# Performance work log

Measured on AMD Instinct MI355X. Metric: run time of the kernel, lower is better.

Reference implementation:

```python
import jax, jax.numpy as jnp
import numpy as np

N_INPUT, N_HIDDEN, N_OUTPUT = 64, 1024, 64
B, T = 128, 512

def setup_inputs() -> dict:
    key = jax.random.key(0)
    ks = jax.random.split(key, 8)
    s_in = 1.0 / np.sqrt(N_INPUT)
    s_h = 1.0 / np.sqrt(N_HIDDEN)
    return {
        "x": jax.random.normal(ks[0], (B, T, N_INPUT), jnp.float32),
        "enc_w": jax.random.uniform(ks[1], (N_HIDDEN, N_INPUT), jnp.float32, -s_in, s_in),
        "enc_b": jax.random.uniform(ks[2], (N_HIDDEN,), jnp.float32, -s_in, s_in),
        "rec_w": jax.random.uniform(ks[3], (N_HIDDEN, N_HIDDEN), jnp.float32, -s_h, s_h),
        "fgt_w": jax.random.uniform(ks[4], (N_HIDDEN, N_HIDDEN), jnp.float32, -s_h, s_h),
        "dec_w": jax.random.uniform(ks[5], (N_OUTPUT, N_HIDDEN), jnp.float32, -s_h, s_h),
        "dec_b": jax.random.uniform(ks[6], (N_OUTPUT,), jnp.float32, -s_h, s_h),
        "hinit_w": jax.random.uniform(ks[7], (N_HIDDEN, 1), jnp.float32, -1.0, 1.0),
        "hinit_b": jax.random.uniform(jax.random.fold_in(key, 9), (N_HIDDEN,), jnp.float32, -1.0, 1.0),
    }

def softsign(x):
    return x / (1.0 + jnp.abs(x))

def reference(x, enc_w, enc_b, rec_w, fgt_w, dec_w, dec_b, hinit_w, hinit_b):
    # x: [B, T, I] -> time-major [T, B, I]
    xt = jnp.transpose(x, (1, 0, 2))
    # hidden_init(ones(B,1)) = ones @ hinit_w^T + b = broadcast of column sum
    hidden0 = jnp.broadcast_to(hinit_w[:, 0] + hinit_b, (x.shape[0], hinit_b.shape[0]))
    # Precompute encoder projection for all timesteps (same math, one big GEMM)
    enc_all = jnp.einsum('tbi,hi->tbh', xt, enc_w) + enc_b  # [T, B, H]

    def step(hidden, enc_t):
        forget = jax.nn.sigmoid(hidden @ fgt_w.T)
        hidden_new = softsign(enc_t + hidden @ rec_w.T)
        hidden = (1.0 - forget) * hidden + forget * hidden_new
        out_t = hidden @ dec_w.T + dec_b
        return hidden, out_t

    hidden, output = jax.lax.scan(step, hidden0, enc_all)
    return output, hidden  # output: [T, B, O], hidden: [B, H]
```

## Files before the change

kernel.cpp:

```cpp
#include <hip/hip_runtime.h>

typedef unsigned short u16;

#define NWG 256
#define NT  256
#define TS  512
#define HD  1024
#define BS  128
#define NI  64
#define NO  64
#define XR  16
#define CC  32
#define RCP 17

typedef __attribute__((ext_vector_type(8))) short bf16x8;
typedef __attribute__((ext_vector_type(4))) float f32x4;

__device__ __forceinline__ float bf2f(u16 u) {
    union { unsigned int i; float f; } v; v.i = ((unsigned int)u) << 16; return v.f;
}
__device__ __forceinline__ u16 f2bf(float f) {
    union { float fl; unsigned int i; } v; v.fl = f;
    unsigned int x = v.i;
    return (u16)((x + 0x7fffu + ((x >> 16) & 1u)) >> 16);
}
__device__ __forceinline__ float ldv(const void* p, size_t i, bool isf32) {
    return isf32 ? ((const float*)p)[i] : bf2f(((const u16*)p)[i]);
}

__device__ __forceinline__ unsigned l2_atomic_add(unsigned* p, unsigned v) {
    unsigned old;
    asm volatile("global_atomic_add %0, %1, %2, off sc0\n\t"
                 "s_waitcnt vmcnt(0)"
                 : "=&v"(old) : "v"(p), "v"(v) : "memory");
    return old;
}
__device__ __forceinline__ void l2_atomic_add_nr(unsigned* p, unsigned v) {
    asm volatile("global_atomic_add %0, %1, off" :: "v"(p), "v"(v) : "memory");
}

__device__ __forceinline__ void load_a_frags(const u16* ap, bf16x8* a) {
    asm volatile(
        "global_load_dwordx4 %0, %8, off sc0\n\t"
        "global_load_dwordx4 %1, %8, off offset:64 sc0\n\t"
        "global_load_dwordx4 %2, %8, off offset:128 sc0\n\t"
        "global_load_dwordx4 %3, %8, off offset:192 sc0\n\t"
        "global_load_dwordx4 %4, %8, off offset:256 sc0\n\t"
        "global_load_dwordx4 %5, %8, off offset:320 sc0\n\t"
        "global_load_dwordx4 %6, %8, off offset:384 sc0\n\t"
        "global_load_dwordx4 %7, %8, off offset:448 sc0\n\t"
        "s_waitcnt vmcnt(0)"
        : "=&v"(a[0]), "=&v"(a[1]), "=&v"(a[2]), "=&v"(a[3]),
          "=&v"(a[4]), "=&v"(a[5]), "=&v"(a[6]), "=&v"(a[7])
        : "v"(ap) : "memory");
}

#define MB_STRIDE 16

__global__ __launch_bounds__(NT)
void arnn_xcd(const void* __restrict__ xv,
              const void* __restrict__ encwv,
              const void* __restrict__ encbv,
              const void* __restrict__ recwv,
              const void* __restrict__ fgtwv,
              const void* __restrict__ decwv,
              const void* __restrict__ decbv,
              const void* __restrict__ hinitwv,
              const void* __restrict__ hinitbv,
              void* __restrict__ outv,
              u16* __restrict__ h0buf,
              u16* __restrict__ h1buf,
              unsigned* __restrict__ tickets,
              unsigned* __restrict__ mboxes)
{
    __shared__ short WB[132 * 64 * 8];
    __shared__ float redC[4 * 5 * 16 * RCP];
    __shared__ float hst[XR * CC];
    __shared__ float encbS[CC];
    __shared__ float decbLS[16];
    __shared__ unsigned s_xcd, s_slot;
    __shared__ int s_f32;

    const int tid  = threadIdx.x;
    const int wave = tid >> 6;
    const int lane = tid & 63;
    const int m    = lane & 15;
    const int quad = lane >> 4;

    if (tid == 0) {
        unsigned xcc;
        asm volatile("s_getreg_b32 %0, hwreg(HW_REG_XCC_ID, 0, 4)" : "=s"(xcc));
        xcc &= 7u;
        unsigned slot = l2_atomic_add(tickets + xcc * 16, 1u);
        s_xcd = xcc;
        s_slot = slot & 31u;
        s_f32 = 0;
    }
    __syncthreads();
    {
        float v = bf2f(((const u16*)recwv)[tid]);
        if (!(v >= -1.0f && v <= 1.0f)) s_f32 = 1;
    }
    __syncthreads();
    const bool isf32 = (s_f32 != 0);
    const int xcd  = (int)s_xcd;
    const int slot = (int)s_slot;
    const int b0   = xcd * XR;
    const int j0   = slot * CC;
    const int dt   = slot & 3;
    unsigned* mbX   = mboxes + (size_t)xcd * 32 * MB_STRIDE;
    unsigned* mbOwn = mbX + slot * MB_STRIDE;

    for (int idx = tid; idx < 132 * 64; idx += NT) {
        int ksg = idx >> 6, l = idx & 63, n = l & 15, q = l >> 4;
        int tile, ksl;
        if (ksg < 34)       { tile = 0; ksl = ksg; }
        else if (ksg < 68)  { tile = 1; ksl = ksg - 34; }
        else if (ksg < 100) { tile = 2; ksl = ksg - 68; }
        else                { tile = 3; ksl = ksg - 100; }
        int j = j0 + ((tile & 1) << 4) + n;
        bf16x8 v;
        if (!isf32) {
            const u16* src;
            if (tile < 2) src = (ksl < 32) ? (const u16*)recwv + (size_t)j * HD + ksl * 32 + q * 8
                                           : (const u16*)encwv + (size_t)j * NI + (ksl - 32) * 32 + q * 8;
            else          src = (const u16*)fgtwv + (size_t)j * HD + ksl * 32 + q * 8;
            v = *(const bf16x8*)src;
        } else {
            const float* src;
            if (tile < 2) src = (ksl < 32) ? (const float*)recwv + (size_t)j * HD + ksl * 32 + q * 8
                                           : (const float*)encwv + (size_t)j * NI + (ksl - 32) * 32 + q * 8;
            else          src = (const float*)fgtwv + (size_t)j * HD + ksl * 32 + q * 8;
            #pragma unroll
            for (int i = 0; i < 8; ++i) v[i] = (short)f2bf(src[i]);
        }
        *(bf16x8*)&WB[idx * 8] = v;
    }
    __syncthreads();

    bf16x8 Breg[2][8];
    #pragma unroll
    for (int ks = 0; ks < 8; ++ks) {
        int kb = wave * 8 + ks;
        Breg[0][ks] = *(const bf16x8*)&WB[((0  + kb) * 64 + lane) * 8];
        Breg[1][ks] = *(const bf16x8*)&WB[((34 + kb) * 64 + lane) * 8];
    }
    bf16x8 Ereg[2];
    if (wave < 2) {
        Ereg[0] = *(const bf16x8*)&WB[((32 + wave) * 64 + lane) * 8];
        Ereg[1] = *(const bf16x8*)&WB[((34 + 32 + wave) * 64 + lane) * 8];
    }
    bf16x8 dfr[8];
    {
        int o = 16 * dt + m;
        #pragma unroll
        for (int ks = 0; ks < 8; ++ks) {
            int kb = wave * 256 + ks * 32 + quad * 8;
            if (!isf32) dfr[ks] = *(const bf16x8*)((const u16*)decwv + (size_t)o * HD + kb);
            else {
                const float* src = (const float*)decwv + (size_t)o * HD + kb;
                #pragma unroll
                for (int i = 0; i < 8; ++i) dfr[ks][i] = (short)f2bf(src[i]);
            }
        }
    }
    if (tid < CC) encbS[tid] = ldv(encbv, j0 + tid, isf32);
    if (tid < 16) decbLS[tid] = ldv(decbv, 16 * dt + tid, isf32);
    for (int e = tid; e < XR * CC; e += NT) {
        int r = e >> 5, c = e & 31;
        float v = ldv(hinitwv, j0 + c, isf32) + ldv(hinitbv, j0 + c, isf32);
        hst[e] = v;
        h0buf[(size_t)(b0 + r) * HD + j0 + c] = f2bf(v);
    }
    __syncthreads();
    if (tid < 32) l2_atomic_add_nr(mbX + tid * MB_STRIDE, 1u);

    for (int t = 0; t < TS; ++t) {
        f32x4 acc[5];
        #pragma unroll
        for (int tt = 0; tt < 5; ++tt) acc[tt] = (f32x4){0.f, 0.f, 0.f, 0.f};

        if (wave < 2) {
            bf16x8 xf;
            size_t xb = (size_t)(b0 + m) * (TS * NI) + (size_t)t * NI + wave * 32 + quad * 8;
            if (!isf32) xf = *(const bf16x8*)((const u16*)xv + xb);
            else {
                const float* xp = (const float*)xv + xb;
                #pragma unroll
                for (int i = 0; i < 8; ++i) xf[i] = (short)f2bf(xp[i]);
            }
            acc[0] = __builtin_amdgcn_mfma_f32_16x16x32_bf16(xf, Ereg[0], acc[0], 0, 0, 0);
            acc[1] = __builtin_amdgcn_mfma_f32_16x16x32_bf16(xf, Ereg[1], acc[1], 0, 0, 0);
        }

        if (lane == 0) {
            unsigned target = 32u * (unsigned)(t + 1);
            while (l2_atomic_add(mbOwn, 0u) < target) {}
        }

        const u16* cur = (t & 1) ? h1buf : h0buf;
        u16*       nxt = (t & 1) ? h0buf : h1buf;

        bf16x8 a[8];
        load_a_frags(cur + (size_t)(b0 + m) * HD + wave * 256 + quad * 8, a);

        #pragma unroll
        for (int ks = 0; ks < 8; ++ks) {
            int kb = wave * 8 + ks;
            bf16x8 bf2 = *(const bf16x8*)&WB[((68  + kb) * 64 + lane) * 8];
            bf16x8 bf3 = *(const bf16x8*)&WB[((100 + kb) * 64 + lane) * 8];
            acc[0] = __builtin_amdgcn_mfma_f32_16x16x32_bf16(a[ks], Breg[0][ks], acc[0], 0, 0, 0);
            acc[1] = __builtin_amdgcn_mfma_f32_16x16x32_bf16(a[ks], Breg[1][ks], acc[1], 0, 0, 0);
            acc[2] = __builtin_amdgcn_mfma_f32_16x16x32_bf16(a[ks], bf2,         acc[2], 0, 0, 0);
            acc[3] = __builtin_amdgcn_mfma_f32_16x16x32_bf16(a[ks], bf3,         acc[3], 0, 0, 0);
            acc[4] = __builtin_amdgcn_mfma_f32_16x16x32_bf16(a[ks], dfr[ks],     acc[4], 0, 0, 0);
        }

        #pragma unroll
        for (int tt = 0; tt < 5; ++tt) {
            #pragma unroll
            for (int r = 0; r < 4; ++r)
                redC[((wave * 5 + tt) * 16 + quad * 4 + r) * RCP + m] = acc[tt][r];
        }
        __syncthreads();

        if (slot < 4 && t > 0) {
            int r = tid >> 4, col = tid & 15;
            float o = decbLS[col];
            #pragma unroll
            for (int kq = 0; kq < 4; ++kq)
                o += redC[((kq * 5 + 4) * 16 + r) * RCP + col];
            size_t oi = (size_t)(t - 1) * (BS * NO) + (size_t)(b0 + r) * NO + 16 * dt + col;
            if (isf32) ((float*)outv)[oi] = o; else ((u16*)outv)[oi] = f2bf(o);
        }
        for (int e = tid; e < XR * CC; e += NT) {
            int r = e >> 5, c = e & 31, tl = c >> 4, col = c & 15;
            float pr = encbS[c], pf = 0.f;
            #pragma unroll
            for (int kq = 0; kq < 4; ++kq) {
                pr += redC[((kq * 5 + tl) * 16 + r) * RCP + col];
                pf += redC[((kq * 5 + 2 + tl) * 16 + r) * RCP + col];
            }
            float fg = 1.0f / (1.0f + __expf(-pf));
            float hn = pr / (1.0f + fabsf(pr));
            float h  = hst[e];
            float hv = h + fg * (hn - h);
            hst[e] = hv;
            nxt[(size_t)(b0 + r) * HD + j0 + c] = f2bf(hv);
        }
        __syncthreads();
        if (tid < 32) l2_atomic_add_nr(mbX + tid * MB_STRIDE, 1u);
    }

    if (lane == 0) {
        unsigned target = 32u * (unsigned)(TS + 1);
        while (l2_atomic_add(mbOwn, 0u) < target) {}
    }
    {
        bf16x8 a[8];
        load_a_frags(h0buf + (size_t)(b0 + m) * HD + wave * 256 + quad * 8, a);
        f32x4 ac = (f32x4){0.f, 0.f, 0.f, 0.f};
        #pragma unroll
        for (int ks = 0; ks < 8; ++ks)
            ac = __builtin_amdgcn_mfma_f32_16x16x32_bf16(a[ks], dfr[ks], ac, 0, 0, 0);
        #pragma unroll
        for (int r = 0; r < 4; ++r)
            redC[((wave * 5 + 4) * 16 + quad * 4 + r) * RCP + m] = ac[r];
        __syncthreads();
        if (slot < 4) {
            int r = tid >> 4, col = tid & 15;
            float o = decbLS[col];
            #pragma unroll
            for (int kq = 0; kq < 4; ++kq)
                o += redC[((kq * 5 + 4) * 16 + r) * RCP + col];
            size_t oi = (size_t)511 * (BS * NO) + (size_t)(b0 + r) * NO + 16 * dt + col;
            if (isf32) ((float*)outv)[oi] = o; else ((u16*)outv)[oi] = f2bf(o);
        }
        for (int e = tid; e < XR * CC; e += NT) {
            int r = e >> 5, c = e & 31;
            size_t oi = (size_t)TS * BS * NO + (size_t)(b0 + r) * HD + j0 + c;
            float v = hst[e];
            if (isf32) ((float*)outv)[oi] = v; else ((u16*)outv)[oi] = f2bf(v);
        }
    }
}

extern "C" void kernel_launch(void* const* d_in, const int* in_sizes, int n_in,
                              void* d_out, int out_size, void* d_ws, size_t ws_size,
                              hipStream_t stream) {
    (void)in_sizes; (void)n_in; (void)out_size; (void)ws_size;
    const void* xv       = d_in[0];
    const void* encwv    = d_in[1];
    const void* encbv    = d_in[2];
    const void* recwv    = d_in[3];
    const void* fgtwv    = d_in[4];
    const void* decwv    = d_in[5];
    const void* decbv    = d_in[6];
    const void* hinitwv  = d_in[7];
    const void* hinitbv  = d_in[8];
    void* outv = d_out;

    unsigned* tickets = (unsigned*)d_ws;
    unsigned* mboxes  = (unsigned*)((char*)d_ws + 4096);
    u16* h0buf = (u16*)((char*)d_ws + 524288);
    u16* h1buf = h0buf + (size_t)BS * HD;

    hipMemsetAsync(d_ws, 0, 4096 + 8 * 32 * 64, stream);

    void* args[] = { (void*)&xv, (void*)&encwv, (void*)&encbv, (void*)&recwv,
                     (void*)&fgtwv, (void*)&decwv, (void*)&decbv,
                     (void*)&hinitwv, (void*)&hinitbv,
                     (void*)&outv, (void*)&h0buf, (void*)&h1buf,
                     (void*)&tickets, (void*)&mboxes };
    hipError_t err = hipLaunchCooperativeKernel((void*)arnn_xcd, dim3(NWG), dim3(NT), args, 0, stream);
    if (err != hipSuccess) {
        hipLaunchKernelGGL(arnn_xcd, dim3(NWG), dim3(NT), 0, stream,
                           xv, encwv, encbv, recwv, fgtwv, decwv, decbv,
                           hinitwv, hinitbv, outv, h0buf, h1buf, tickets, mboxes);
    }
}
```

Before: 1.592 ms.

## Split per-XCD batch into two 8-row groups with per-producer flag mailboxes

Each workgroup now processes its 16 batch rows as two groups of 8, each with its own barrier, so work on one group can overlap other workgroups still finishing the other group. The shared atomic counter is replaced by a per-producer flag array: each producer writes its own slot and consumers poll all 32 flags with a wave-wide vote. Forget-gate weights are kept in registers instead of being reloaded from LDS each step, and decoder MFMAs run only on the 4 decoder workgroups. The catch is that each MFMA now uses only 8 of its 16 rows, which doubles MFMA and reduction passes per step, and register pressure goes up.

```diff
diff --git a/kernel.cpp b/kernel.cpp
--- a/kernel.cpp
+++ b/kernel.cpp
@@ -9,9 +9,11 @@
 #define BS  128
 #define NI  64
 #define NO  64
-#define XR  16
+#define GR  2
+#define GXR 8
 #define CC  32
 #define RCP 17
+#define MBW 32
 
 typedef __attribute__((ext_vector_type(8))) short bf16x8;
 typedef __attribute__((ext_vector_type(4))) float f32x4;
@@ -34,9 +36,6 @@
                  "s_waitcnt vmcnt(0)"
                  : "=&v"(old) : "v"(p), "v"(v) : "memory");
     return old;
-}
-__device__ __forceinline__ void l2_atomic_add_nr(unsigned* p, unsigned v) {
-    asm volatile("global_atomic_add %0, %1, off" :: "v"(p), "v"(v) : "memory");
 }
 
 __device__ __forceinline__ void load_a_frags(const u16* ap, bf16x8* a) {
@@ -55,7 +54,6 @@
         : "v"(ap) : "memory");
 }
 
-#define MB_STRIDE 16
 
 __global__ __launch_bounds__(NT)
 void arnn_xcd(const void* __restrict__ xv,
@@ -75,9 +73,6 @@
 {
     __shared__ short WB[132 * 64 * 8];
     __shared__ float redC[4 * 5 * 16 * RCP];
-    __shared__ float hst[XR * CC];
-    __shared__ float encbS[CC];
-    __shared__ float decbLS[16];
     __shared__ unsigned s_xcd, s_slot;
     __shared__ int s_f32;
 
@@ -105,11 +100,11 @@
     const bool isf32 = (s_f32 != 0);
     const int xcd  = (int)s_xcd;
     const int slot = (int)s_slot;
-    const int b0   = xcd * XR;
+    const int b0   = xcd * (GR * GXR);
     const int j0   = slot * CC;
     const int dt   = slot & 3;
-    unsigned* mbX   = mboxes + (size_t)xcd * 32 * MB_STRIDE;
-    unsigned* mbOwn = mbX + slot * MB_STRIDE;
+    const bool dec_cu = (slot < 4);
+    unsigned* mbX = mboxes + (size_t)xcd * GR * 32 * MBW;
 
     for (int idx = tid; idx < 132 * 64; idx += NT) {
         int ksg = idx >> 6, l = idx & 63, n = l & 15, q = l >> 4;
@@ -139,11 +134,14 @@
     __syncthreads();
 
     bf16x8 Breg[2][8];
+    bf16x8 Freg[2][8];
     #pragma unroll
     for (int ks = 0; ks < 8; ++ks) {
         int kb = wave * 8 + ks;
-        Breg[0][ks] = *(const bf16x8*)&WB[((0  + kb) * 64 + lane) * 8];
-        Breg[1][ks] = *(const bf16x8*)&WB[((34 + kb) * 64 + lane) * 8];
+        Breg[0][ks] = *(const bf16x8*)&WB[((0   + kb) * 64 + lane) * 8];
+        Breg[1][ks] = *(const bf16x8*)&WB[((34  + kb) * 64 + lane) * 8];
+        Freg[0][ks] = *(const bf16x8*)&WB[((68  + kb) * 64 + lane) * 8];
+        Freg[1][ks] = *(const bf16x8*)&WB[((100 + kb) * 64 + lane) * 8];
     }
     bf16x8 Ereg[2];
     if (wave < 2) {
@@ -164,124 +162,146 @@
             }
         }
     }
-    if (tid < CC) encbS[tid] = ldv(encbv, j0 + tid, isf32);
-    if (tid < 16) decbLS[tid] = ldv(decbv, 16 * dt + tid, isf32);
-    for (int e = tid; e < XR * CC; e += NT) {
-        int r = e >> 5, c = e & 31;
-        float v = ldv(hinitwv, j0 + c, isf32) + ldv(hinitbv, j0 + c, isf32);
-        hst[e] = v;
-        h0buf[(size_t)(b0 + r) * HD + j0 + c] = f2bf(v);
-    }
+    const int er = tid >> 5, ec = tid & 31;
+    float encb_r = ldv(encbv, j0 + ec, isf32);
+    float decb_r = ldv(decbv, 16 * dt + (tid & 15), isf32);
+    float h0v = ldv(hinitwv, j0 + ec, isf32) + ldv(hinitbv, j0 + ec, isf32);
+    float hst0 = h0v, hst1 = h0v;
+    h0buf[(size_t)(b0 +       er) * HD + j0 + ec] = f2bf(h0v);
+    h0buf[(size_t)(b0 + GXR + er) * HD + j0 + ec] = f2bf(h0v);
     __syncthreads();
-    if (tid < 32) l2_atomic_add_nr(mbX + tid * MB_STRIDE, 1u);
+    if (tid < 32) {
+        ((volatile unsigned*)mbX)[0 * 32 * MBW + tid * MBW + slot] = 1u;
+        ((volatile unsigned*)mbX)[1 * 32 * MBW + tid * MBW + slot] = 1u;
+    }
 
     for (int t = 0; t < TS; ++t) {
-        f32x4 acc[5];
-        #pragma unroll
-        for (int tt = 0; tt < 5; ++tt) acc[tt] = (f32x4){0.f, 0.f, 0.f, 0.f};
-
-        if (wave < 2) {
-            bf16x8 xf;
-            size_t xb = (size_t)(b0 + m) * (TS * NI) + (size_t)t * NI + wave * 32 + quad * 8;
-            if (!isf32) xf = *(const bf16x8*)((const u16*)xv + xb);
-            else {
-                const float* xp = (const float*)xv + xb;
-                #pragma unroll
-                for (int i = 0; i < 8; ++i) xf[i] = (short)f2bf(xp[i]);
-            }
-            acc[0] = __builtin_amdgcn_mfma_f32_16x16x32_bf16(xf, Ereg[0], acc[0], 0, 0, 0);
-            acc[1] = __builtin_amdgcn_mfma_f32_16x16x32_bf16(xf, Ereg[1], acc[1], 0, 0, 0);
-        }
-
-        if (lane == 0) {
-            unsigned target = 32u * (unsigned)(t + 1);
-            while (l2_atomic_add(mbOwn, 0u) < target) {}
-        }
-
         const u16* cur = (t & 1) ? h1buf : h0buf;
         u16*       nxt = (t & 1) ? h0buf : h1buf;
-
-        bf16x8 a[8];
-        load_a_frags(cur + (size_t)(b0 + m) * HD + wave * 256 + quad * 8, a);
-
         #pragma unroll
-        for (int ks = 0; ks < 8; ++ks) {
-            int kb = wave * 8 + ks;
-            bf16x8 bf2 = *(const bf16x8*)&WB[((68  + kb) * 64 + lane) * 8];
-            bf16x8 bf3 = *(const bf16x8*)&WB[((100 + kb) * 64 + lane) * 8];
-            acc[0] = __builtin_amdgcn_mfma_f32_16x16x32_bf16(a[ks], Breg[0][ks], acc[0], 0, 0, 0);
-            acc[1] = __builtin_amdgcn_mfma_f32_16x16x32_bf16(a[ks], Breg[1][ks], acc[1], 0, 0, 0);
-            acc[2] = __builtin_amdgcn_mfma_f32_16x16x32_bf16(a[ks], bf2,         acc[2], 0, 0, 0);
-            acc[3] = __builtin_amdgcn_mfma_f32_16x16x32_bf16(a[ks], bf3,         acc[3], 0, 0, 0);
-            acc[4] = __builtin_amdgcn_mfma_f32_16x16x32_bf16(a[ks], dfr[ks],     acc[4], 0, 0, 0);
-        }
-
-        #pragma unroll
-        for (int tt = 0; tt < 5; ++tt) {
+        for (int g = 0; g < GR; ++g) {
+            f32x4 acc[5];
+            #pragma unroll
+            for (int tt = 0; tt < 5; ++tt) acc[tt] = (f32x4){0.f, 0.f, 0.f, 0.f};
+
+            if (wave < 2) {
+                bf16x8 xf;
+                size_t xb = (size_t)(b0 + g * GXR + (m & 7)) * (TS * NI) + (size_t)t * NI + wave * 32 + quad * 8;
+                if (!isf32) xf = *(const bf16x8*)((const u16*)xv + xb);
+                else {
+                    const float* xp = (const float*)xv + xb;
+                    #pragma unroll
+                    for (int i = 0; i < 8; ++i) xf[i] = (short)f2bf(xp[i]);
+                }
+                acc[0] = __builtin_amdgcn_mfma_f32_16x16x32_bf16(xf, Ereg[0], acc[0], 0, 0, 0);
+                acc[1] = __builtin_amdgcn_mfma_f32_16x16x32_bf16(xf, Ereg[1], acc[1], 0, 0, 0);
+            }
+
+            {
+                const unsigned target = (unsigned)(t + 1);
+                unsigned* pb = mbX + g * 32 * MBW + slot * MBW;
+                for (;;) {
+                    unsigned v = 0xFFFFFFFFu;
+                    if (lane < 32) v = l2_atomic_add(pb + lane, 0u);
+                    if (__all((int)(v >= target))) break;
+                }
+            }
+
+            bf16x8 a[8];
+            load_a_frags(cur + (size_t)(b0 + g * GXR + (m & 7)) * HD + wave * 256 + quad * 8, a);
+
+            #pragma unroll
+            for (int ks = 0; ks < 8; ++ks) {
+                acc[0] = __builtin_amdgcn_mfma_f32_16x16x32_bf16(a[ks], Breg[0][ks], acc[0], 0, 0, 0);
+                acc[1] = __builtin_amdgcn_mfma_f32_16x16x32_bf16(a[ks], Breg[1][ks], acc[1], 0, 0, 0);
+                acc[2] = __builtin_amdgcn_mfma_f32_16x16x32_bf16(a[ks], Freg[0][ks], acc[2], 0, 0, 0);
+                acc[3] = __builtin_amdgcn_mfma_f32_16x16x32_bf16(a[ks], Freg[1][ks], acc[3], 0, 0, 0);
+            }
+            if (dec_cu) {
+                #pragma unroll
+                for (int ks = 0; ks < 8; ++ks)
+                    acc[4] = __builtin_amdgcn_mfma_f32_16x16x32_bf16(a[ks], dfr[ks], acc[4], 0, 0, 0);
+            }
+
+            #pragma unroll
+            for (int tt = 0; tt < 4; ++tt) {
+                #pragma unroll
+                for (int r = 0; r < 4; ++r)
+                    redC[((wave * 5 + tt) * 16 + quad * 4 + r) * RCP + m] = acc[tt][r];
+            }
+            if (dec_cu) {
+                #pragma unroll
+                for (int r = 0; r < 4; ++r)
+                    redC[((wave * 5 + 4) * 16 + quad * 4 + r) * RCP + m] = acc[4][r];
+            }
+            __syncthreads();
+
+            if (dec_cu && t > 0 && tid < 128) {
+                int r = tid >> 4, col = tid & 15;
+                float o = decb_r;
+                #pragma unroll
+                for (int kq = 0; kq < 4; ++kq)
+                    o += redC[((kq * 5 + 4) * 16 + r) * RCP + col];
+                size_t oi = (size_t)(t - 1) * (BS * NO) + (size_t)(b0 + g * GXR + r) * NO + 16 * dt + col;
+                if (isf32) ((float*)outv)[oi] = o; else ((u16*)outv)[oi] = f2bf(o);
+            }
+            {
+                const int tl = ec >> 4, col = ec & 15;
+                float pr = encb_r, pf = 0.f;
+                #pragma unroll
+                for (int kq = 0; kq < 4; ++kq) {
+                    pr += redC[((kq * 5 + tl) * 16 + er) * RCP + col];
+                    pf += redC[((kq * 5 + 2 + tl) * 16 + er) * RCP + col];
+                }
+                float fg = 1.0f / (1.0f + __expf(-pf));
+                float hn = pr / (1.0f + fabsf(pr));
+                float h  = (g == 0) ? hst0 : hst1;
+                float hv = h + fg * (hn - h);
+                if (g == 0) hst0 = hv; else hst1 = hv;
+                nxt[(size_t)(b0 + g * GXR + er) * HD + j0 + ec] = f2bf(hv);
+            }
+            __syncthreads();
+            if (tid < 32)
+                ((volatile unsigned*)mbX)[g * 32 * MBW + tid * MBW + slot] = (unsigned)(t + 2);
+        }
+    }
+
+    #pragma unroll
+    for (int g = 0; g < GR; ++g) {
+        if (dec_cu) {
+            const unsigned target = (unsigned)(TS + 1);
+            unsigned* pb = mbX + g * 32 * MBW + slot * MBW;
+            for (;;) {
+                unsigned v = 0xFFFFFFFFu;
+                if (lane < 32) v = l2_atomic_add(pb + lane, 0u);
+                if (__all((int)(v >= target))) break;
+            }
+            bf16x8 a[8];
+            load_a_frags(h0buf + (size_t)(b0 + g * GXR + (m & 7)) * HD + wave * 256 + quad * 8, a);
+            f32x4 ac = (f32x4){0.f, 0.f, 0.f, 0.f};
+            #pragma unroll
+            for (int ks = 0; ks < 8; ++ks)
+                ac = __builtin_amdgcn_mfma_f32_16x16x32_bf16(a[ks], dfr[ks], ac, 0, 0, 0);
             #pragma unroll
             for (int r = 0; r < 4; ++r)
-                redC[((wave * 5 + tt) * 16 + quad * 4 + r) * RCP + m] = acc[tt][r];
+                redC[((wave * 5 + 4) * 16 + quad * 4 + r) * RCP + m] = ac[r];
         }
         __syncthreads();
-
-        if (slot < 4 && t > 0) {
+        if (dec_cu && tid < 128) {
             int r = tid >> 4, col = tid & 15;
-            float o = decbLS[col];
+            float o = decb_r;
             #pragma unroll
             for (int kq = 0; kq < 4; ++kq)
                 o += redC[((kq * 5 + 4) * 16 + r) * RCP + col];
-            size_t oi = (size_t)(t - 1) * (BS * NO) + (size_t)(b0 + r) * NO + 16 * dt + col;
+            size_t oi = (size_t)511 * (BS * NO) + (size_t)(b0 + g * GXR + r) * NO + 16 * dt + col;
             if (isf32) ((float*)outv)[oi] = o; else ((u16*)outv)[oi] = f2bf(o);
         }
-        for (int e = tid; e < XR * CC; e += NT) {
-            int r = e >> 5, c = e & 31, tl = c >> 4, col = c & 15;
-            float pr = encbS[c], pf = 0.f;
-            #pragma unroll
-            for (int kq = 0; kq < 4; ++kq) {
-                pr += redC[((kq * 5 + tl) * 16 + r) * RCP + col];
-                pf += redC[((kq * 5 + 2 + tl) * 16 + r) * RCP + col];
-            }
-            float fg = 1.0f / (1.0f + __expf(-pf));
-            float hn = pr / (1.0f + fabsf(pr));
-            float h  = hst[e];
-            float hv = h + fg * (hn - h);
-            hst[e] = hv;
-            nxt[(size_t)(b0 + r) * HD + j0 + c] = f2bf(hv);
+        {
+            size_t oi = (size_t)TS * BS * NO + (size_t)(b0 + g * GXR + er) * HD + j0 + ec;
+            float v = (g == 0) ? hst0 : hst1;
+            if (isf32) ((float*)outv)[oi] = v; else ((u16*)outv)[oi] = f2bf(v);
         }
         __syncthreads();
-        if (tid < 32) l2_atomic_add_nr(mbX + tid * MB_STRIDE, 1u);
-    }
-
-    if (lane == 0) {
-        unsigned target = 32u * (unsigned)(TS + 1);
-        while (l2_atomic_add(mbOwn, 0u) < target) {}
-    }
-    {
-        bf16x8 a[8];
-        load_a_frags(h0buf + (size_t)(b0 + m) * HD + wave * 256 + quad * 8, a);
-        f32x4 ac = (f32x4){0.f, 0.f, 0.f, 0.f};
-        #pragma unroll
-        for (int ks = 0; ks < 8; ++ks)
-            ac = __builtin_amdgcn_mfma_f32_16x16x32_bf16(a[ks], dfr[ks], ac, 0, 0, 0);
-        #pragma unroll
-        for (int r = 0; r < 4; ++r)
-            redC[((wave * 5 + 4) * 16 + quad * 4 + r) * RCP + m] = ac[r];
-        __syncthreads();
-        if (slot < 4) {
-            int r = tid >> 4, col = tid & 15;
-            float o = decbLS[col];
-            #pragma unroll
-            for (int kq = 0; kq < 4; ++kq)
-                o += redC[((kq * 5 + 4) * 16 + r) * RCP + col];
-            size_t oi = (size_t)511 * (BS * NO) + (size_t)(b0 + r) * NO + 16 * dt + col;
-            if (isf32) ((float*)outv)[oi] = o; else ((u16*)outv)[oi] = f2bf(o);
-        }
-        for (int e = tid; e < XR * CC; e += NT) {
-            int r = e >> 5, c = e & 31;
-            size_t oi = (size_t)TS * BS * NO + (size_t)(b0 + r) * HD + j0 + c;
-            float v = hst[e];
-            if (isf32) ((float*)outv)[oi] = v; else ((u16*)outv)[oi] = f2bf(v);
-        }
     }
 }
 
@@ -305,7 +325,7 @@
     u16* h0buf = (u16*)((char*)d_ws + 524288);
     u16* h1buf = h0buf + (size_t)BS * HD;
 
-    hipMemsetAsync(d_ws, 0, 4096 + 8 * 32 * 64, stream);
+    hipMemsetAsync(d_ws, 0, 4096 + GR * 8 * 32 * MBW * 4, stream);
 
     void* args[] = { (void*)&xv, (void*)&encwv, (void*)&encbv, (void*)&recwv,
                      (void*)&fgtwv, (void*)&decwv, (void*)&decbv,
```

Result: slower. 2.394 ms (+50.3%).
